# Kernel optimization log

Hardware: AMD Instinct MI355X
Metric: run time of the kernel (lower is better)

## Reference

```python
import jax, jax.numpy as jnp
import numpy as np

B, T, P, V, D, DINO, H, L = 32, 40, 256, 4096, 256, 384, 4, 2
HD = D // H          # head dim 64
DFF = 4 * D          # 1024
EPS = 1e-5


def setup_inputs() -> dict:
    key = jax.random.key(0)
    ks = iter(jax.random.split(key, 40))
    rn = lambda shape, s=0.02: jax.random.normal(next(ks), shape, jnp.float32) * s
    return dict(
        patches=jax.random.normal(next(ks), (B, P, DINO), jnp.float32),
        tokens=jax.random.randint(next(ks), (B, T), 0, V, jnp.int32),
        tok_emb=rn((V, D)),
        pos_emb=rn((1, T, D)),
        qkv_w=rn((L, 3 * D, D)), qkv_b=jnp.zeros((L, 3 * D), jnp.float32),
        out_w=rn((L, D, D)), out_b=jnp.zeros((L, D), jnp.float32),
        ln1_s=jnp.ones((L, D), jnp.float32), ln1_b=jnp.zeros((L, D), jnp.float32),
        w1=rn((L, DFF, D)), b1=jnp.zeros((L, DFF), jnp.float32),
        w2=rn((L, D, DFF)), b2=jnp.zeros((L, D), jnp.float32),
        ln2_s=jnp.ones((L, D), jnp.float32), ln2_b=jnp.zeros((L, D), jnp.float32),
        fus_w1=rn((D, DINO + D)), fus_b1=jnp.zeros((D,), jnp.float32),
        fus_w2=rn((D, D)), fus_b2=jnp.zeros((D,), jnp.float32),
        cls_w=rn((V, D)), cls_b=jnp.zeros((V,), jnp.float32),
    )


def _ln(x, s, b):
    m = jnp.mean(x, -1, keepdims=True)
    v = jnp.var(x, -1, keepdims=True)
    return (x - m) * jax.lax.rsqrt(v + EPS) * s + b


def _token_encoder(tokens, tok_emb, pos_emb, qkv_w, qkv_b, out_w, out_b,
                   ln1_s, ln1_b, w1, b1, w2, b2, ln2_s, ln2_b):
    # Causal full-sequence pass: output at position t equals re-running the
    # unmasked encoder on tokens[:, :t+1] and taking the last position.
    x = tok_emb[tokens] + pos_emb[:, :tokens.shape[1], :]   # [B,T,D]
    causal = jnp.triu(jnp.full((T, T), -1e9, jnp.float32), 1)  # [T,T]
    for l in range(L):  # fixed small layer count
        qkv = x @ qkv_w[l].T + qkv_b[l]                     # [B,T,3D]
        q, k, v = jnp.split(qkv, 3, axis=-1)
        q = q.reshape(B, T, H, HD).transpose(0, 2, 1, 3)    # [B,H,T,hd]
        k = k.reshape(B, T, H, HD).transpose(0, 2, 1, 3)
        v = v.reshape(B, T, H, HD).transpose(0, 2, 1, 3)
        scores = jnp.einsum('bhqd,bhkd->bhqk', q, k) / np.sqrt(HD).astype(np.float32)
        attn = jax.nn.softmax(scores + causal, axis=-1)
        ctx = jnp.einsum('bhqk,bhkd->bhqd', attn, v)        # [B,H,T,hd]
        ctx = ctx.transpose(0, 2, 1, 3).reshape(B, T, D)
        x = _ln(x + ctx @ out_w[l].T + out_b[l], ln1_s[l], ln1_b[l])
        h = jax.nn.relu(x @ w1[l].T + b1[l]) @ w2[l].T + b2[l]
        x = _ln(x + h, ln2_s[l], ln2_b[l])
    return x  # [B,T,D]


def reference(patches, tokens, tok_emb, pos_emb, qkv_w, qkv_b, out_w, out_b,
              ln1_s, ln1_b, w1, b1, w2, b2, ln2_s, ln2_b,
              fus_w1, fus_b1, fus_w2, fus_b2, cls_w, cls_b):
    enc = _token_encoder(tokens, tok_emb, pos_emb, qkv_w, qkv_b, out_w, out_b,
                         ln1_s, ln1_b, w1, b1, w2, b2, ln2_s, ln2_b)  # [B,T,D]
    # context for step 0 is zeros; step t>0 uses encoder output at position t-1
    ctx = jnp.concatenate([jnp.zeros((B, 1, D), enc.dtype), enc[:, :-1]], axis=1)  # [B,T,D]
    # fusion MLP: split the concat-linear into a patch part and a context part
    wp, wc = fus_w1[:, :DINO], fus_w1[:, DINO:]
    pproj = patches @ wp.T                                  # [B,P,D]
    cproj = ctx @ wc.T + fus_b1                             # [B,T,D]
    h = jax.nn.gelu(pproj[:, None, :, :] + cproj[:, :, None, :], approximate=False)  # [B,T,P,D]
    fused = h @ fus_w2.T + fus_b2                           # [B,T,P,D]
    # sigmoid+gather of the 4096-way logits == gather classifier rows, dot, sigmoid
    w_sel = cls_w[tokens]                                   # [B,T,D]
    b_sel = cls_b[tokens]                                   # [B,T]
    logits = jnp.einsum('btpd,btd->btp', fused, w_sel) + b_sel[:, :, None]
    probs = jax.nn.sigmoid(logits)                          # [B,T,P]
    return probs.transpose(0, 2, 1)                         # [B,P,T] == [B,256,40]
```

## Files before the change

kernel.cpp:

```cpp
#include <hip/hip_runtime.h>
#include <hip/hip_bf16.h>

#define B_ 32
#define T_ 40
#define P_ 256
#define V_ 4096
#define D_ 256
#define DINO_ 384
#define H_ 4
#define L_ 2
#define HD_ 64
#define DFF_ 1024
#define EPS_ 1e-5f

typedef __bf16 bf16;
typedef __bf16 bf16x8 __attribute__((ext_vector_type(8)));
typedef float f32x4 __attribute__((ext_vector_type(4)));

#define OFF_QKV 0
#define OFF_OUTW 393216
#define OFF_W1 524288
#define OFF_W2 1048576
#define OFF_FUS 1572864
#define WB_TOTAL 1736704
#define CONV_BLOCKS 848

__device__ __forceinline__ bf16x8 cvt8(const float* p) {
  float4 f0 = *(const float4*)p;
  float4 f1 = *(const float4*)(p + 4);
  bf16x8 v;
  v[0] = (bf16)f0.x; v[1] = (bf16)f0.y; v[2] = (bf16)f0.z; v[3] = (bf16)f0.w;
  v[4] = (bf16)f1.x; v[5] = (bf16)f1.y; v[6] = (bf16)f1.z; v[7] = (bf16)f1.w;
  return v;
}

__global__ __launch_bounds__(256) void prep_k(
    const int* __restrict__ tokens, const float* __restrict__ tok_emb,
    const float* __restrict__ pos_emb, float* __restrict__ x,
    const float* __restrict__ fus_w2, bf16* __restrict__ w2Tb,
    const float* __restrict__ qkv_w, const float* __restrict__ out_w,
    const float* __restrict__ w1, const float* __restrict__ w2,
    const float* __restrict__ fus_w1, bf16* __restrict__ wb) {
  __shared__ float tile[32][33];
  int bi = blockIdx.x;
  int tid = threadIdx.x;
  if (bi < B_ * T_) {
    int t = bi % T_;
    x[bi * D_ + tid] = tok_emb[tokens[bi] * D_ + tid] + pos_emb[t * D_ + tid];
  } else if (bi < B_ * T_ + 64) {
    int tt = bi - B_ * T_;
    int bx = (tt & 7) * 32, by = (tt >> 3) * 32;
    int tx = tid & 31, ty = tid >> 5;
#pragma unroll
    for (int i = 0; i < 32; i += 8) tile[ty + i][tx] = fus_w2[(by + ty + i) * D_ + bx + tx];
    __syncthreads();
#pragma unroll
    for (int i = 0; i < 32; i += 8)
      w2Tb[(bx + ty + i) * D_ + by + tx] = (bf16)tile[tx][ty + i];
  } else {
    long f = (long)(bi - B_ * T_ - 64) * 2048 + tid * 8;
    const float* src;
    long off;
    if (f < OFF_OUTW)      { src = qkv_w;  off = f - OFF_QKV; }
    else if (f < OFF_W1)   { src = out_w;  off = f - OFF_OUTW; }
    else if (f < OFF_W2)   { src = w1;     off = f - OFF_W1; }
    else if (f < OFF_FUS)  { src = w2;     off = f - OFF_W2; }
    else                   { src = fus_w1; off = f - OFF_FUS; }
    *(bf16x8*)&wb[f] = cvt8(src + off);
  }
}

__global__ __launch_bounds__(256) void gemm_k(
    const float* __restrict__ A, const bf16* __restrict__ W,
    const float* __restrict__ bias, float* __restrict__ out,
    int K, int lda, int ldw, int ldc, int relu) {
  __shared__ bf16 As[32 * 72];
  __shared__ bf16 Ws[32 * 72];
  const int tid = threadIdx.x;
  const int lane = tid & 63;
  const int wv = tid >> 6;
  const int mi = wv & 1, ni = wv >> 1;
  const int col = lane & 15;
  const int quad = lane >> 4;
  const int bn = blockIdx.x * 32;
  const int bm = blockIdx.y * 32;
  const int srow = tid >> 3;
  const int kc = (tid & 7) * 8;
  const float* Ap = A + (long)(bm + srow) * lda;
  const bf16* Wp = W + (long)(bn + srow) * ldw;

  f32x4 acc = {0.f, 0.f, 0.f, 0.f};
  for (int kk = 0; kk < K; kk += 64) {
    *(bf16x8*)&As[srow * 72 + kc] = cvt8(Ap + kk + kc);
    *(bf16x8*)&Ws[srow * 72 + kc] = *(const bf16x8*)(Wp + kk + kc);
    __syncthreads();
#pragma unroll
    for (int ki = 0; ki < 2; ++ki) {
      bf16x8 afr = *(const bf16x8*)&As[(mi * 16 + col) * 72 + ki * 32 + quad * 8];
      bf16x8 bfr = *(const bf16x8*)&Ws[(ni * 16 + col) * 72 + ki * 32 + quad * 8];
      acc = __builtin_amdgcn_mfma_f32_16x16x32_bf16(afr, bfr, acc, 0, 0, 0);
    }
    __syncthreads();
  }
  const int n = bn + ni * 16 + col;
  float bv = bias ? bias[n] : 0.0f;
#pragma unroll
  for (int r = 0; r < 4; ++r) {
    int m = bm + mi * 16 + quad * 4 + r;
    float val = acc[r] + bv;
    if (relu) val = fmaxf(val, 0.0f);
    out[(long)m * ldc + n] = val;
  }
}

__global__ __launch_bounds__(256) void fuse3_k(
    const float* __restrict__ patches, const float* __restrict__ xbuf,
    const float* __restrict__ cls_w, const bf16* __restrict__ fusb,
    const bf16* __restrict__ w2Tb, const float* __restrict__ fus_b1,
    const int* __restrict__ tokens, float* __restrict__ pprojT,
    float* __restrict__ cw) {
  __shared__ bf16 As[32 * 72];
  __shared__ bf16 Ws[32 * 72];
  const int tid = threadIdx.x;
  const int lane = tid & 63;
  const int wv = tid >> 6;
  const int mi = wv & 1, ni = wv >> 1;
  const int col = lane & 15;
  const int quad = lane >> 4;
  const int bn = blockIdx.x * 32;
  const int y = blockIdx.y;
  const int srow = tid >> 3;
  const int kc = (tid & 7) * 8;

  int job, bm;
  if (y < 256) { job = 0; bm = y * 32; }
  else if (y < 296) { job = 1; bm = (y - 256) * 32; }
  else { job = 2; bm = (y - 296) * 32; }
  const int gm = bm + srow;

  const float* Ap;
  const bf16* Wp;
  int K;
  bool zeroA = false;
  if (job == 0) {
    Ap = patches + (long)gm * DINO_;
    Wp = fusb + (long)(bn + srow) * 640;
    K = DINO_;
  } else if (job == 1) {
    int t = gm % T_;
    zeroA = (t == 0);
    Ap = xbuf + (long)(zeroA ? gm : gm - 1) * D_;
    Wp = fusb + 384 + (long)(bn + srow) * 640;
    K = D_;
  } else {
    Ap = cls_w + (long)tokens[gm] * D_;
    Wp = w2Tb + (long)(bn + srow) * D_;
    K = D_;
  }

  f32x4 acc = {0.f, 0.f, 0.f, 0.f};
  bf16x8 z8 = {};
  for (int kk = 0; kk < K; kk += 64) {
    bf16x8 av = zeroA ? z8 : cvt8(Ap + kk + kc);
    *(bf16x8*)&As[srow * 72 + kc] = av;
    *(bf16x8*)&Ws[srow * 72 + kc] = *(const bf16x8*)(Wp + kk + kc);
    __syncthreads();
#pragma unroll
    for (int ki = 0; ki < 2; ++ki) {
      bf16x8 afr = *(const bf16x8*)&As[(mi * 16 + col) * 72 + ki * 32 + quad * 8];
      bf16x8 bfr = *(const bf16x8*)&Ws[(ni * 16 + col) * 72 + ki * 32 + quad * 8];
      acc = __builtin_amdgcn_mfma_f32_16x16x32_bf16(afr, bfr, acc, 0, 0, 0);
    }
    __syncthreads();
  }
  const int n = bn + ni * 16 + col;
  if (job == 0) {
#pragma unroll
    for (int r = 0; r < 4; ++r) {
      int m = bm + mi * 16 + quad * 4 + r;
      int b = m >> 8, p = m & 255;
      pprojT[(long)b * (D_ * P_) + (long)n * P_ + p] = acc[r];
    }
  } else if (job == 1) {
    float bv = fus_b1[n];
#pragma unroll
    for (int r = 0; r < 4; ++r) {
      int m = bm + mi * 16 + quad * 4 + r;
      cw[(long)m * (2 * D_) + n * 2] = acc[r] + bv;
    }
  } else {
#pragma unroll
    for (int r = 0; r < 4; ++r) {
      int m = bm + mi * 16 + quad * 4 + r;
      cw[(long)m * (2 * D_) + n * 2 + 1] = acc[r];
    }
  }
}

__global__ __launch_bounds__(256) void attn_k(const float* __restrict__ qkv,
                                              float* __restrict__ ctx) {
  __shared__ float q[T_][HD_ + 1];
  __shared__ float k[T_][HD_ + 1];
  __shared__ float v[T_][HD_ + 1];
  __shared__ float s[T_][T_ + 1];
  int h = blockIdx.x, b = blockIdx.y;
  int tid = threadIdx.x;
  for (int idx = tid; idx < T_ * HD_; idx += 256) {
    int t = idx >> 6, d = idx & 63;
    long base = (long)(b * T_ + t) * (3 * D_) + h * HD_ + d;
    q[t][d] = qkv[base];
    k[t][d] = qkv[base + D_];
    v[t][d] = qkv[base + 2 * D_];
  }
  __syncthreads();
  for (int idx = tid; idx < T_ * T_; idx += 256) {
    int i = idx / T_, j = idx - i * T_;
    if (j <= i) {
      float acc = 0.f;
#pragma unroll
      for (int d = 0; d < HD_; ++d) acc += q[i][d] * k[j][d];
      s[i][j] = acc * 0.125f;
    }
  }
  __syncthreads();
  if (tid < T_) {
    int i = tid;
    float mx = -1e30f;
    for (int j = 0; j <= i; ++j) mx = fmaxf(mx, s[i][j]);
    float sum = 0.f;
    for (int j = 0; j <= i; ++j) {
      float e = __expf(s[i][j] - mx);
      s[i][j] = e;
      sum += e;
    }
    float inv = 1.0f / sum;
    for (int j = 0; j <= i; ++j) s[i][j] *= inv;
  }
  __syncthreads();
  for (int idx = tid; idx < T_ * HD_; idx += 256) {
    int i = idx >> 6, d = idx & 63;
    float acc = 0.f;
    for (int j = 0; j <= i; ++j) acc += s[i][j] * v[j][d];
    ctx[(long)(b * T_ + i) * D_ + h * HD_ + d] = acc;
  }
}

__global__ __launch_bounds__(256) void ln_k(float* __restrict__ x, const float* __restrict__ y,
                                            const float* __restrict__ g,
                                            const float* __restrict__ be) {
  __shared__ float red[4];
  int m = blockIdx.x, d = threadIdx.x;
  int lane = d & 63, wv = d >> 6;
  float val = x[m * D_ + d] + y[m * D_ + d];
  float sv = val;
#pragma unroll
  for (int mk = 1; mk < 64; mk <<= 1) sv += __shfl_xor(sv, mk);
  if (lane == 0) red[wv] = sv;
  __syncthreads();
  float mean = (red[0] + red[1] + red[2] + red[3]) * (1.0f / D_);
  __syncthreads();
  float c = val - mean;
  float s2 = c * c;
#pragma unroll
  for (int mk = 1; mk < 64; mk <<= 1) s2 += __shfl_xor(s2, mk);
  if (lane == 0) red[wv] = s2;
  __syncthreads();
  float var = (red[0] + red[1] + red[2] + red[3]) * (1.0f / D_);
  x[m * D_ + d] = c * rsqrtf(var + EPS_) * g[d] + be[d];
}

__global__ __launch_bounds__(256) void final_k(const float* __restrict__ pprojT,
                                               const float* __restrict__ cw,
                                               const int* __restrict__ tokens,
                                               const float* __restrict__ cls_w,
                                               const float* __restrict__ cls_b,
                                               const float* __restrict__ fus_b2,
                                               float* __restrict__ out) {
  int lane = threadIdx.x & 63, wv = threadIdx.x >> 6;
  int p = blockIdx.x * 64 + lane;
  int t = blockIdx.y * 4 + wv;
  int b = blockIdx.z;
  int m = b * T_ + t;
  int tok = tokens[m];
  const float* cr = cls_w + (long)tok * D_;
  float bacc = 0.f;
#pragma unroll
  for (int i = 0; i < 4; ++i) bacc += cr[lane + i * 64] * fus_b2[lane + i * 64];
#pragma unroll
  for (int mk = 1; mk < 64; mk <<= 1) bacc += __shfl_xor(bacc, mk);
  float beff = bacc + cls_b[tok];

  const float* ppb = pprojT + (long)b * (D_ * P_);
  const float* cwt = cw + (long)m * (D_ * 2);
  float acc = 0.f;
#pragma unroll 8
  for (int e = 0; e < D_; ++e) {
    float pp = ppb[e * P_ + p];
    float2 c = *(const float2*)&cwt[e * 2];
    float x = pp + c.x;
    float x2 = x * x;
    float u = x * fmaf(-0.1029432f, x2, -2.3022083f);
    float ex = __builtin_amdgcn_exp2f(u);
    float r = __builtin_amdgcn_rcpf(1.0f + ex);
    acc = fmaf(x * r, c.y, acc);
  }
  float logit = acc + beff;
  float es = __builtin_amdgcn_exp2f(-1.4426950408889634f * logit);
  out[(long)(b * P_ + p) * T_ + t] = __builtin_amdgcn_rcpf(1.0f + es);
}

extern "C" void kernel_launch(void* const* d_in, const int* in_sizes, int n_in, void* d_out,
                              int out_size, void* d_ws, size_t ws_size, hipStream_t stream) {
  const float* patches = (const float*)d_in[0];
  const int* tokens = (const int*)d_in[1];
  const float* tok_emb = (const float*)d_in[2];
  const float* pos_emb = (const float*)d_in[3];
  const float* qkv_w = (const float*)d_in[4];
  const float* qkv_b = (const float*)d_in[5];
  const float* out_w = (const float*)d_in[6];
  const float* out_b = (const float*)d_in[7];
  const float* ln1_s = (const float*)d_in[8];
  const float* ln1_b = (const float*)d_in[9];
  const float* w1 = (const float*)d_in[10];
  const float* b1 = (const float*)d_in[11];
  const float* w2 = (const float*)d_in[12];
  const float* b2 = (const float*)d_in[13];
  const float* ln2_s = (const float*)d_in[14];
  const float* ln2_b = (const float*)d_in[15];
  const float* fus_w1 = (const float*)d_in[16];
  const float* fus_b1 = (const float*)d_in[17];
  const float* fus_w2 = (const float*)d_in[18];
  const float* fus_b2 = (const float*)d_in[19];
  const float* cls_w = (const float*)d_in[20];
  const float* cls_b = (const float*)d_in[21];
  float* out = (float*)d_out;

  float* xbuf = (float*)d_ws;
  float* qkvbuf = xbuf + B_ * T_ * D_;
  float* tmp = qkvbuf + B_ * T_ * 3 * D_;
  float* hbuf = tmp + B_ * T_ * D_;
  float* pprojT = hbuf + B_ * T_ * DFF_;
  float* cwbuf = pprojT + (long)B_ * D_ * P_;
  bf16* wb = (bf16*)(cwbuf + B_ * T_ * D_ * 2);
  bf16* w2Tb = wb + WB_TOTAL;

  const int MT = B_ * T_;

  prep_k<<<MT + 64 + CONV_BLOCKS, 256, 0, stream>>>(
      tokens, tok_emb, pos_emb, xbuf, fus_w2, w2Tb, qkv_w, out_w, w1, w2, fus_w1, wb);

  for (int l = 0; l < L_; ++l) {
    gemm_k<<<dim3(24, 40), 256, 0, stream>>>(
        xbuf, wb + OFF_QKV + (long)l * 3 * D_ * D_, qkv_b + l * 3 * D_, qkvbuf,
        D_, D_, D_, 3 * D_, 0);
    attn_k<<<dim3(H_, B_), 256, 0, stream>>>(qkvbuf, hbuf);
    gemm_k<<<dim3(8, 40), 256, 0, stream>>>(
        hbuf, wb + OFF_OUTW + (long)l * D_ * D_, out_b + l * D_, tmp,
        D_, D_, D_, D_, 0);
    ln_k<<<MT, D_, 0, stream>>>(xbuf, tmp, ln1_s + l * D_, ln1_b + l * D_);
    gemm_k<<<dim3(32, 40), 256, 0, stream>>>(
        xbuf, wb + OFF_W1 + (long)l * DFF_ * D_, b1 + l * DFF_, hbuf,
        D_, D_, D_, DFF_, 1);
    gemm_k<<<dim3(8, 40), 256, 0, stream>>>(
        hbuf, wb + OFF_W2 + (long)l * D_ * DFF_, b2 + l * D_, tmp,
        DFF_, DFF_, DFF_, D_, 0);
    ln_k<<<MT, D_, 0, stream>>>(xbuf, tmp, ln2_s + l * D_, ln2_b + l * D_);
  }

  fuse3_k<<<dim3(8, 336), 256, 0, stream>>>(patches, xbuf, cls_w, wb + OFF_FUS, w2Tb,
                                            fus_b1, tokens, pprojT, cwbuf);

  final_k<<<dim3(4, 10, 32), 256, 0, stream>>>(pprojT, cwbuf, tokens, cls_w, cls_b,
                                               fus_b2, out);
}
```

Before: 269.8 us.

## Fuse LayerNorm and residual into GEMM prologues/epilogues, drop ln_k launches

```diff
diff --git a/kernel.cpp b/kernel.cpp
--- a/kernel.cpp
+++ b/kernel.cpp
@@ -24,6 +24,7 @@
 #define OFF_FUS 1572864
 #define WB_TOTAL 1736704
 #define CONV_BLOCKS 848
+#define PAT_BLOCKS 1536
 
 __device__ __forceinline__ bf16x8 cvt8(const float* p) {
   float4 f0 = *(const float4*)p;
@@ -40,7 +41,8 @@
     const float* __restrict__ fus_w2, bf16* __restrict__ w2Tb,
     const float* __restrict__ qkv_w, const float* __restrict__ out_w,
     const float* __restrict__ w1, const float* __restrict__ w2,
-    const float* __restrict__ fus_w1, bf16* __restrict__ wb) {
+    const float* __restrict__ fus_w1, bf16* __restrict__ wb,
+    const float* __restrict__ patches, bf16* __restrict__ patb) {
   __shared__ float tile[32][33];
   int bi = blockIdx.x;
   int tid = threadIdx.x;
@@ -57,7 +59,7 @@
 #pragma unroll
     for (int i = 0; i < 32; i += 8)
       w2Tb[(bx + ty + i) * D_ + by + tx] = (bf16)tile[tx][ty + i];
-  } else {
+  } else if (bi < B_ * T_ + 64 + CONV_BLOCKS) {
     long f = (long)(bi - B_ * T_ - 64) * 2048 + tid * 8;
     const float* src;
     long off;
@@ -67,132 +69,233 @@
     else if (f < OFF_FUS)  { src = w2;     off = f - OFF_W2; }
     else                   { src = fus_w1; off = f - OFF_FUS; }
     *(bf16x8*)&wb[f] = cvt8(src + off);
-  }
-}
-
+  } else {
+    long f = (long)(bi - B_ * T_ - 64 - CONV_BLOCKS) * 2048 + tid * 8;
+    *(bf16x8*)&patb[f] = cvt8(patches + f);
+  }
+}
+
+template <int ALN, int ABF16, int OBF16, int RELU, int RESID, int WLN>
 __global__ __launch_bounds__(256) void gemm_k(
-    const float* __restrict__ A, const bf16* __restrict__ W,
-    const float* __restrict__ bias, float* __restrict__ out,
-    int K, int lda, int ldw, int ldc, int relu) {
-  __shared__ bf16 As[32 * 72];
+    const void* __restrict__ Av, const bf16* __restrict__ W,
+    const float* __restrict__ bias, const float* __restrict__ lng,
+    const float* __restrict__ lnb, const float* __restrict__ resid,
+    float* __restrict__ xlnout, void* __restrict__ outv,
+    int K, int lda, int ldw, int ldc) {
+  __shared__ bf16 As[32 * 264];
   __shared__ bf16 Ws[32 * 72];
   const int tid = threadIdx.x;
   const int lane = tid & 63;
   const int wv = tid >> 6;
   const int mi = wv & 1, ni = wv >> 1;
-  const int col = lane & 15;
-  const int quad = lane >> 4;
-  const int bn = blockIdx.x * 32;
-  const int bm = blockIdx.y * 32;
-  const int srow = tid >> 3;
-  const int kc = (tid & 7) * 8;
-  const float* Ap = A + (long)(bm + srow) * lda;
-  const bf16* Wp = W + (long)(bn + srow) * ldw;
-
+  const int col = lane & 15, quad = lane >> 4;
+  const int bn = blockIdx.x * 32, bm = blockIdx.y * 32;
+  const int srow = tid >> 3, kc = (tid & 7) * 8;
+  const bf16* Wp = W + (long)(bn + srow) * ldw + kc;
   f32x4 acc = {0.f, 0.f, 0.f, 0.f};
-  for (int kk = 0; kk < K; kk += 64) {
-    *(bf16x8*)&As[srow * 72 + kc] = cvt8(Ap + kk + kc);
-    *(bf16x8*)&Ws[srow * 72 + kc] = *(const bf16x8*)(Wp + kk + kc);
+
+  if (ALN) {
+    const float* S = (const float*)Av;
+    const int r = srow, cg = (tid & 7) * 32;
+    const float* sp = S + (long)(bm + r) * lda + cg;
+    float v[32];
+    float sum = 0.f, ss = 0.f;
+#pragma unroll
+    for (int i = 0; i < 8; ++i) {
+      float4 f = *(const float4*)(sp + i * 4);
+      v[i*4] = f.x; v[i*4+1] = f.y; v[i*4+2] = f.z; v[i*4+3] = f.w;
+      sum += f.x + f.y + f.z + f.w;
+      ss += f.x*f.x + f.y*f.y + f.z*f.z + f.w*f.w;
+    }
+#pragma unroll
+    for (int mk = 1; mk < 8; mk <<= 1) {
+      sum += __shfl_xor(sum, mk);
+      ss += __shfl_xor(ss, mk);
+    }
+    float mean = sum * (1.0f / D_);
+    float inv = rsqrtf(ss * (1.0f / D_) - mean * mean + EPS_);
+#pragma unroll
+    for (int i = 0; i < 8; ++i) {
+      float4 g4 = *(const float4*)(lng + cg + i * 4);
+      float4 b4 = *(const float4*)(lnb + cg + i * 4);
+      float n0 = (v[i*4]   - mean) * inv * g4.x + b4.x;
+      float n1 = (v[i*4+1] - mean) * inv * g4.y + b4.y;
+      float n2 = (v[i*4+2] - mean) * inv * g4.z + b4.z;
+      float n3 = (v[i*4+3] - mean) * inv * g4.w + b4.w;
+      As[r * 264 + cg + i*4]     = (bf16)n0;
+      As[r * 264 + cg + i*4 + 1] = (bf16)n1;
+      As[r * 264 + cg + i*4 + 2] = (bf16)n2;
+      As[r * 264 + cg + i*4 + 3] = (bf16)n3;
+      if (WLN) {
+        if (blockIdx.x == 0) {
+          float4 o; o.x = n0; o.y = n1; o.z = n2; o.w = n3;
+          *(float4*)&xlnout[(long)(bm + r) * D_ + cg + i*4] = o;
+        }
+      }
+    }
     __syncthreads();
-#pragma unroll
-    for (int ki = 0; ki < 2; ++ki) {
-      bf16x8 afr = *(const bf16x8*)&As[(mi * 16 + col) * 72 + ki * 32 + quad * 8];
-      bf16x8 bfr = *(const bf16x8*)&Ws[(ni * 16 + col) * 72 + ki * 32 + quad * 8];
-      acc = __builtin_amdgcn_mfma_f32_16x16x32_bf16(afr, bfr, acc, 0, 0, 0);
-    }
-    __syncthreads();
-  }
+    for (int kk = 0; kk < 256; kk += 64) {
+      *(bf16x8*)&Ws[srow * 72 + kc] = *(const bf16x8*)(Wp + kk);
+      __syncthreads();
+#pragma unroll
+      for (int ki = 0; ki < 2; ++ki) {
+        bf16x8 afr = *(const bf16x8*)&As[(mi*16 + col) * 264 + kk + ki*32 + quad*8];
+        bf16x8 bfr = *(const bf16x8*)&Ws[(ni*16 + col) * 72 + ki*32 + quad*8];
+        acc = __builtin_amdgcn_mfma_f32_16x16x32_bf16(afr, bfr, acc, 0, 0, 0);
+      }
+      __syncthreads();
+    }
+  } else {
+    const float* Af = (const float*)Av;
+    const bf16* Ab = (const bf16*)Av;
+    for (int kk = 0; kk < K; kk += 64) {
+      if (ABF16)
+        *(bf16x8*)&As[srow * 72 + kc] = *(const bf16x8*)(Ab + (long)(bm + srow) * lda + kk + kc);
+      else
+        *(bf16x8*)&As[srow * 72 + kc] = cvt8(Af + (long)(bm + srow) * lda + kk + kc);
+      *(bf16x8*)&Ws[srow * 72 + kc] = *(const bf16x8*)(Wp + kk);
+      __syncthreads();
+#pragma unroll
+      for (int ki = 0; ki < 2; ++ki) {
+        bf16x8 afr = *(const bf16x8*)&As[(mi*16 + col) * 72 + ki*32 + quad*8];
+        bf16x8 bfr = *(const bf16x8*)&Ws[(ni*16 + col) * 72 + ki*32 + quad*8];
+        acc = __builtin_amdgcn_mfma_f32_16x16x32_bf16(afr, bfr, acc, 0, 0, 0);
+      }
+      __syncthreads();
+    }
+  }
+
   const int n = bn + ni * 16 + col;
   float bv = bias ? bias[n] : 0.0f;
 #pragma unroll
-  for (int r = 0; r < 4; ++r) {
-    int m = bm + mi * 16 + quad * 4 + r;
-    float val = acc[r] + bv;
-    if (relu) val = fmaxf(val, 0.0f);
-    out[(long)m * ldc + n] = val;
+  for (int r4 = 0; r4 < 4; ++r4) {
+    int m = bm + mi * 16 + quad * 4 + r4;
+    float val = acc[r4] + bv;
+    if (RESID) val += resid[(long)m * D_ + n];
+    if (RELU) val = fmaxf(val, 0.0f);
+    if (OBF16) ((bf16*)outv)[(long)m * ldc + n] = (bf16)val;
+    else ((float*)outv)[(long)m * ldc + n] = val;
   }
 }
 
 __global__ __launch_bounds__(256) void fuse3_k(
-    const float* __restrict__ patches, const float* __restrict__ xbuf,
+    const bf16* __restrict__ patb, const float* __restrict__ s2,
+    const float* __restrict__ lng, const float* __restrict__ lnb,
     const float* __restrict__ cls_w, const bf16* __restrict__ fusb,
     const bf16* __restrict__ w2Tb, const float* __restrict__ fus_b1,
     const int* __restrict__ tokens, float* __restrict__ pprojT,
     float* __restrict__ cw) {
-  __shared__ bf16 As[32 * 72];
+  __shared__ bf16 As[32 * 264];
   __shared__ bf16 Ws[32 * 72];
   const int tid = threadIdx.x;
   const int lane = tid & 63;
   const int wv = tid >> 6;
   const int mi = wv & 1, ni = wv >> 1;
-  const int col = lane & 15;
-  const int quad = lane >> 4;
+  const int col = lane & 15, quad = lane >> 4;
   const int bn = blockIdx.x * 32;
   const int y = blockIdx.y;
-  const int srow = tid >> 3;
-  const int kc = (tid & 7) * 8;
+  const int srow = tid >> 3, kc = (tid & 7) * 8;
 
   int job, bm;
   if (y < 256) { job = 0; bm = y * 32; }
   else if (y < 296) { job = 1; bm = (y - 256) * 32; }
   else { job = 2; bm = (y - 296) * 32; }
-  const int gm = bm + srow;
-
-  const float* Ap;
-  const bf16* Wp;
-  int K;
-  bool zeroA = false;
-  if (job == 0) {
-    Ap = patches + (long)gm * DINO_;
-    Wp = fusb + (long)(bn + srow) * 640;
-    K = DINO_;
-  } else if (job == 1) {
-    int t = gm % T_;
-    zeroA = (t == 0);
-    Ap = xbuf + (long)(zeroA ? gm : gm - 1) * D_;
-    Wp = fusb + 384 + (long)(bn + srow) * 640;
-    K = D_;
+
+  f32x4 acc = {0.f, 0.f, 0.f, 0.f};
+
+  if (job == 1) {
+    const int r = srow, cg = (tid & 7) * 32;
+    const int gm = bm + r;
+    const int t = gm % T_;
+    if (t == 0) {
+      bf16x8 z8 = {};
+#pragma unroll
+      for (int i = 0; i < 4; ++i) *(bf16x8*)&As[r * 264 + cg + i * 8] = z8;
+    } else {
+      const float* sp = s2 + (long)(gm - 1) * D_ + cg;
+      float v[32];
+      float sum = 0.f, ss = 0.f;
+#pragma unroll
+      for (int i = 0; i < 8; ++i) {
+        float4 f = *(const float4*)(sp + i * 4);
+        v[i*4] = f.x; v[i*4+1] = f.y; v[i*4+2] = f.z; v[i*4+3] = f.w;
+        sum += f.x + f.y + f.z + f.w;
+        ss += f.x*f.x + f.y*f.y + f.z*f.z + f.w*f.w;
+      }
+#pragma unroll
+      for (int mk = 1; mk < 8; mk <<= 1) {
+        sum += __shfl_xor(sum, mk);
+        ss += __shfl_xor(ss, mk);
+      }
+      float mean = sum * (1.0f / D_);
+      float inv = rsqrtf(ss * (1.0f / D_) - mean * mean + EPS_);
+#pragma unroll
+      for (int i = 0; i < 8; ++i) {
+        float4 g4 = *(const float4*)(lng + cg + i * 4);
+        float4 b4 = *(const float4*)(lnb + cg + i * 4);
+        As[r*264 + cg + i*4]     = (bf16)((v[i*4]   - mean) * inv * g4.x + b4.x);
+        As[r*264 + cg + i*4 + 1] = (bf16)((v[i*4+1] - mean) * inv * g4.y + b4.y);
+        As[r*264 + cg + i*4 + 2] = (bf16)((v[i*4+2] - mean) * inv * g4.z + b4.z);
+        As[r*264 + cg + i*4 + 3] = (bf16)((v[i*4+3] - mean) * inv * g4.w + b4.w);
+      }
+    }
+    __syncthreads();
+    const bf16* Wp = fusb + 384 + (long)(bn + srow) * 640 + kc;
+    for (int kk = 0; kk < 256; kk += 64) {
+      *(bf16x8*)&Ws[srow * 72 + kc] = *(const bf16x8*)(Wp + kk);
+      __syncthreads();
+#pragma unroll
+      for (int ki = 0; ki < 2; ++ki) {
+        bf16x8 afr = *(const bf16x8*)&As[(mi*16 + col) * 264 + kk + ki*32 + quad*8];
+        bf16x8 bfr = *(const bf16x8*)&Ws[(ni*16 + col) * 72 + ki*32 + quad*8];
+        acc = __builtin_amdgcn_mfma_f32_16x16x32_bf16(afr, bfr, acc, 0, 0, 0);
+      }
+      __syncthreads();
+    }
   } else {
-    Ap = cls_w + (long)tokens[gm] * D_;
-    Wp = w2Tb + (long)(bn + srow) * D_;
-    K = D_;
-  }
-
-  f32x4 acc = {0.f, 0.f, 0.f, 0.f};
-  bf16x8 z8 = {};
-  for (int kk = 0; kk < K; kk += 64) {
-    bf16x8 av = zeroA ? z8 : cvt8(Ap + kk + kc);
-    *(bf16x8*)&As[srow * 72 + kc] = av;
-    *(bf16x8*)&Ws[srow * 72 + kc] = *(const bf16x8*)(Wp + kk + kc);
-    __syncthreads();
-#pragma unroll
-    for (int ki = 0; ki < 2; ++ki) {
-      bf16x8 afr = *(const bf16x8*)&As[(mi * 16 + col) * 72 + ki * 32 + quad * 8];
-      bf16x8 bfr = *(const bf16x8*)&Ws[(ni * 16 + col) * 72 + ki * 32 + quad * 8];
-      acc = __builtin_amdgcn_mfma_f32_16x16x32_bf16(afr, bfr, acc, 0, 0, 0);
-    }
-    __syncthreads();
-  }
+    const bf16* Wp;
+    int K;
+    if (job == 0) { Wp = fusb + (long)(bn + srow) * 640 + kc; K = DINO_; }
+    else          { Wp = w2Tb + (long)(bn + srow) * D_ + kc;  K = D_; }
+    for (int kk = 0; kk < K; kk += 64) {
+      if (job == 0)
+        *(bf16x8*)&As[srow * 72 + kc] =
+            *(const bf16x8*)(patb + (long)(bm + srow) * DINO_ + kk + kc);
+      else
+        *(bf16x8*)&As[srow * 72 + kc] =
+            cvt8(cls_w + (long)tokens[bm + srow] * D_ + kk + kc);
+      *(bf16x8*)&Ws[srow * 72 + kc] = *(const bf16x8*)(Wp + kk);
+      __syncthreads();
+#pragma unroll
+      for (int ki = 0; ki < 2; ++ki) {
+        bf16x8 afr = *(const bf16x8*)&As[(mi*16 + col) * 72 + ki*32 + quad*8];
+        bf16x8 bfr = *(const bf16x8*)&Ws[(ni*16 + col) * 72 + ki*32 + quad*8];
+        acc = __builtin_amdgcn_mfma_f32_16x16x32_bf16(afr, bfr, acc, 0, 0, 0);
+      }
+      __syncthreads();
+    }
+  }
+
   const int n = bn + ni * 16 + col;
   if (job == 0) {
 #pragma unroll
-    for (int r = 0; r < 4; ++r) {
-      int m = bm + mi * 16 + quad * 4 + r;
+    for (int r4 = 0; r4 < 4; ++r4) {
+      int m = bm + mi * 16 + quad * 4 + r4;
       int b = m >> 8, p = m & 255;
-      pprojT[(long)b * (D_ * P_) + (long)n * P_ + p] = acc[r];
+      pprojT[(long)b * (D_ * P_) + (long)n * P_ + p] = acc[r4];
     }
   } else if (job == 1) {
     float bv = fus_b1[n];
 #pragma unroll
-    for (int r = 0; r < 4; ++r) {
-      int m = bm + mi * 16 + quad * 4 + r;
-      cw[(long)m * (2 * D_) + n * 2] = acc[r] + bv;
+    for (int r4 = 0; r4 < 4; ++r4) {
+      int m = bm + mi * 16 + quad * 4 + r4;
+      cw[(long)m * (2 * D_) + n * 2] = acc[r4] + bv;
     }
   } else {
 #pragma unroll
-    for (int r = 0; r < 4; ++r) {
-      int m = bm + mi * 16 + quad * 4 + r;
-      cw[(long)m * (2 * D_) + n * 2 + 1] = acc[r];
+    for (int r4 = 0; r4 < 4; ++r4) {
+      int m = bm + mi * 16 + quad * 4 + r4;
+      cw[(long)m * (2 * D_) + n * 2 + 1] = acc[r4];
     }
   }
 }
@@ -245,30 +348,6 @@
   }
 }
 
-__global__ __launch_bounds__(256) void ln_k(float* __restrict__ x, const float* __restrict__ y,
-                                            const float* __restrict__ g,
-                                            const float* __restrict__ be) {
-  __shared__ float red[4];
-  int m = blockIdx.x, d = threadIdx.x;
-  int lane = d & 63, wv = d >> 6;
-  float val = x[m * D_ + d] + y[m * D_ + d];
-  float sv = val;
-#pragma unroll
-  for (int mk = 1; mk < 64; mk <<= 1) sv += __shfl_xor(sv, mk);
-  if (lane == 0) red[wv] = sv;
-  __syncthreads();
-  float mean = (red[0] + red[1] + red[2] + red[3]) * (1.0f / D_);
-  __syncthreads();
-  float c = val - mean;
-  float s2 = c * c;
-#pragma unroll
-  for (int mk = 1; mk < 64; mk <<= 1) s2 += __shfl_xor(s2, mk);
-  if (lane == 0) red[wv] = s2;
-  __syncthreads();
-  float var = (red[0] + red[1] + red[2] + red[3]) * (1.0f / D_);
-  x[m * D_ + d] = c * rsqrtf(var + EPS_) * g[d] + be[d];
-}
-
 __global__ __launch_bounds__(256) void final_k(const float* __restrict__ pprojT,
                                                const float* __restrict__ cw,
                                                const int* __restrict__ tokens,
@@ -276,10 +355,19 @@
                                                const float* __restrict__ cls_b,
                                                const float* __restrict__ fus_b2,
                                                float* __restrict__ out) {
-  int lane = threadIdx.x & 63, wv = threadIdx.x >> 6;
+  __shared__ float2 cws[4][D_];
+  int tid = threadIdx.x;
+  int lane = tid & 63, wv = tid >> 6;
   int p = blockIdx.x * 64 + lane;
   int t = blockIdx.y * 4 + wv;
   int b = blockIdx.z;
+  int mbase = b * T_ + blockIdx.y * 4;
+  for (int idx = tid; idx < 4 * D_; idx += 256) {
+    int tt = idx >> 8, e = idx & 255;
+    cws[tt][e] = ((const float2*)cw)[(long)(mbase + tt) * D_ + e];
+  }
+  __syncthreads();
+
   int m = b * T_ + t;
   int tok = tokens[m];
   const float* cr = cls_w + (long)tok * D_;
@@ -291,12 +379,11 @@
   float beff = bacc + cls_b[tok];
 
   const float* ppb = pprojT + (long)b * (D_ * P_);
-  const float* cwt = cw + (long)m * (D_ * 2);
   float acc = 0.f;
 #pragma unroll 8
   for (int e = 0; e < D_; ++e) {
     float pp = ppb[e * P_ + p];
-    float2 c = *(const float2*)&cwt[e * 2];
+    float2 c = cws[wv][e];
     float x = pp + c.x;
     float x2 = x * x;
     float u = x * fmaf(-0.1029432f, x2, -2.3022083f);
@@ -335,40 +422,52 @@
   const float* cls_b = (const float*)d_in[21];
   float* out = (float*)d_out;
 
-  float* xbuf = (float*)d_ws;
-  float* qkvbuf = xbuf + B_ * T_ * D_;
-  float* tmp = qkvbuf + B_ * T_ * 3 * D_;
-  float* hbuf = tmp + B_ * T_ * D_;
-  float* pprojT = hbuf + B_ * T_ * DFF_;
+  const int MT = B_ * T_;
+  float* x0 = (float*)d_ws;
+  float* qkvbuf = x0 + MT * D_;
+  float* attbuf = qkvbuf + MT * 3 * D_;
+  float* s1 = attbuf + MT * D_;
+  float* xln1 = s1 + MT * D_;
+  float* s2 = xln1 + MT * D_;
+  float* xln2 = s2 + MT * D_;
+  float* pprojT = xln2 + MT * D_;
   float* cwbuf = pprojT + (long)B_ * D_ * P_;
-  bf16* wb = (bf16*)(cwbuf + B_ * T_ * D_ * 2);
+  bf16* wb = (bf16*)(cwbuf + MT * D_ * 2);
   bf16* w2Tb = wb + WB_TOTAL;
-
-  const int MT = B_ * T_;
-
-  prep_k<<<MT + 64 + CONV_BLOCKS, 256, 0, stream>>>(
-      tokens, tok_emb, pos_emb, xbuf, fus_w2, w2Tb, qkv_w, out_w, w1, w2, fus_w1, wb);
+  bf16* patb = w2Tb + D_ * D_;
+  bf16* hb = patb + (long)B_ * P_ * DINO_;
+
+  prep_k<<<MT + 64 + CONV_BLOCKS + PAT_BLOCKS, 256, 0, stream>>>(
+      tokens, tok_emb, pos_emb, x0, fus_w2, w2Tb, qkv_w, out_w, w1, w2, fus_w1, wb,
+      patches, patb);
 
   for (int l = 0; l < L_; ++l) {
-    gemm_k<<<dim3(24, 40), 256, 0, stream>>>(
-        xbuf, wb + OFF_QKV + (long)l * 3 * D_ * D_, qkv_b + l * 3 * D_, qkvbuf,
-        D_, D_, D_, 3 * D_, 0);
-    attn_k<<<dim3(H_, B_), 256, 0, stream>>>(qkvbuf, hbuf);
-    gemm_k<<<dim3(8, 40), 256, 0, stream>>>(
-        hbuf, wb + OFF_OUTW + (long)l * D_ * D_, out_b + l * D_, tmp,
-        D_, D_, D_, D_, 0);
-    ln_k<<<MT, D_, 0, stream>>>(xbuf, tmp, ln1_s + l * D_, ln1_b + l * D_);
-    gemm_k<<<dim3(32, 40), 256, 0, stream>>>(
-        xbuf, wb + OFF_W1 + (long)l * DFF_ * D_, b1 + l * DFF_, hbuf,
-        D_, D_, D_, DFF_, 1);
-    gemm_k<<<dim3(8, 40), 256, 0, stream>>>(
-        hbuf, wb + OFF_W2 + (long)l * D_ * DFF_, b2 + l * D_, tmp,
-        DFF_, DFF_, DFF_, D_, 0);
-    ln_k<<<MT, D_, 0, stream>>>(xbuf, tmp, ln2_s + l * D_, ln2_b + l * D_);
-  }
-
-  fuse3_k<<<dim3(8, 336), 256, 0, stream>>>(patches, xbuf, cls_w, wb + OFF_FUS, w2Tb,
-                                            fus_b1, tokens, pprojT, cwbuf);
+    const float* xin = (l == 0) ? x0 : s2;
+    const float* presid = (l == 0) ? x0 : xln2;
+    if (l == 0) {
+      gemm_k<0,0,0,0,0,0><<<dim3(24, 40), 256, 0, stream>>>(
+          x0, wb + OFF_QKV, qkv_b, nullptr, nullptr, nullptr, nullptr, qkvbuf,
+          D_, D_, D_, 3 * D_);
+    } else {
+      gemm_k<1,0,0,0,0,1><<<dim3(24, 40), 256, 0, stream>>>(
+          s2, wb + OFF_QKV + (long)l * 3 * D_ * D_, qkv_b + l * 3 * D_,
+          ln2_s, ln2_b, nullptr, xln2, qkvbuf, D_, D_, D_, 3 * D_);
+    }
+    attn_k<<<dim3(H_, B_), 256, 0, stream>>>(qkvbuf, attbuf);
+    gemm_k<0,0,0,0,1,0><<<dim3(8, 40), 256, 0, stream>>>(
+        attbuf, wb + OFF_OUTW + (long)l * D_ * D_, out_b + l * D_,
+        nullptr, nullptr, presid, nullptr, s1, D_, D_, D_, D_);
+    gemm_k<1,0,1,1,0,1><<<dim3(32, 40), 256, 0, stream>>>(
+        s1, wb + OFF_W1 + (long)l * DFF_ * D_, b1 + l * DFF_,
+        ln1_s + l * D_, ln1_b + l * D_, nullptr, xln1, hb, D_, D_, D_, DFF_);
+    gemm_k<0,1,0,0,1,0><<<dim3(8, 40), 256, 0, stream>>>(
+        hb, wb + OFF_W2 + (long)l * D_ * DFF_, b2 + l * D_,
+        nullptr, nullptr, xln1, nullptr, s2, DFF_, DFF_, DFF_, D_);
+  }
+
+  fuse3_k<<<dim3(8, 336), 256, 0, stream>>>(patb, s2, ln2_s + D_, ln2_b + D_, cls_w,
+                                            wb + OFF_FUS, w2Tb, fus_b1, tokens,
+                                            pprojT, cwbuf);
 
   final_k<<<dim3(4, 10, 32), 256, 0, stream>>>(pprojT, cwbuf, tokens, cls_w, cls_b,
                                                fus_b2, out);
```

After: 298.7 us. 1.11x slower.
